# Performance work log

Measured on AMD Instinct MI355X. Metric: run time of the kernel, lower is better.

Reference implementation:

```python
import jax, jax.numpy as jnp
import numpy as np

B, S, D = 4, 4096, 1024
E, H, TOPK = 8, 2752, 2


def setup_inputs() -> dict:
    key = jax.random.key(0)
    k0, k1, k2, k3, k4 = jax.random.split(key, 5)
    x = jax.random.normal(k0, (B, S, D), dtype=jnp.float32)
    gate_w = jax.random.normal(k1, (E, D), dtype=jnp.float32) * 0.02
    w1 = jax.random.normal(k2, (E, H, D), dtype=jnp.float32) * 0.02
    w2 = jax.random.normal(k3, (E, D, H), dtype=jnp.float32) * 0.02
    w3 = jax.random.normal(k4, (E, H, D), dtype=jnp.float32) * 0.02
    return {"x": x, "gate_w": gate_w, "w1": w1, "w2": w2, "w3": w3}


def reference(x, gate_w, w1, w2, w3):
    """MoE layer: softmax router -> top-k (normalized) -> per-expert SwiGLU FFN -> weighted combine."""
    b, s, d = x.shape
    xt = x.reshape(-1, d)                       # [T, D], T = B*S
    logits = xt @ gate_w.T                      # [T, E]
    scores = jax.nn.softmax(logits, axis=-1)
    topk_w, topk_i = jax.lax.top_k(scores, TOPK)  # [T, K]
    topk_w = topk_w / (jnp.sum(topk_w, axis=-1, keepdims=True) + 1e-20)

    y = jnp.zeros_like(xt)
    n_experts = gate_w.shape[0]
    for e in range(n_experts):
        # combine weight for expert e per token (0 if not routed to e)
        we = jnp.sum(jnp.where(topk_i == e, topk_w, 0.0), axis=-1)  # [T]
        h = jax.nn.silu(xt @ w1[e].T) * (xt @ w3[e].T)              # [T, H]
        y = y + we[:, None] * (h @ w2[e].T)                         # [T, D]
    return y.reshape(b, s, d)
```

## Files before the change

### kernel.cpp

```cpp
#include <hip/hip_runtime.h>
#include <hip/hip_bf16.h>
#include <stdint.h>

#define T_TOK 16384
#define D_DIM 1024
#define E_NUM 8
#define H_DIM 2752
#define NSLOT (T_TOK * 2)

typedef __bf16 bf16x8_t __attribute__((ext_vector_type(8)));
typedef float f32x4_t __attribute__((ext_vector_type(4)));

__device__ __forceinline__ uint16_t f2bf(float f) {
    union { float f; uint32_t u; } v; v.f = f;
    return (uint16_t)((v.u + 0x7FFFu + ((v.u >> 16) & 1u)) >> 16);
}
__device__ __forceinline__ ushort4 f4_to_bf4(float4 v) {
    ushort4 r; r.x = f2bf(v.x); r.y = f2bf(v.y); r.z = f2bf(v.z); r.w = f2bf(v.w);
    return r;
}
__device__ __forceinline__ void gl_lds16(const uint16_t* g, uint16_t* l) {
    __builtin_amdgcn_global_load_lds((const __attribute__((address_space(1))) void*)g,
                                     (__attribute__((address_space(3))) void*)l,
                                     16, 0, 0);
}

__global__ __launch_bounds__(256) void router_kernel(
    const float* __restrict__ x, const float* __restrict__ gw,
    int* __restrict__ topk_i, float* __restrict__ topk_w) {
    int tid = threadIdx.x;
    int t = blockIdx.x * 4 + (tid >> 6);
    int lane = tid & 63;
    const float* xr = x + (size_t)t * D_DIM;
    double acc[E_NUM];
#pragma unroll
    for (int e = 0; e < E_NUM; ++e) acc[e] = 0.0;
    for (int k = lane; k < D_DIM; k += 64) {
        double xv = (double)xr[k];
#pragma unroll
        for (int e = 0; e < E_NUM; ++e) acc[e] += xv * (double)gw[e * D_DIM + k];
    }
#pragma unroll
    for (int e = 0; e < E_NUM; ++e) {
        double v = acc[e];
        for (int off = 32; off > 0; off >>= 1) v += __shfl_down(v, off, 64);
        acc[e] = v;
    }
    if (lane == 0) {
        int i0 = 0; double m0 = acc[0];
#pragma unroll
        for (int e = 1; e < E_NUM; ++e) if (acc[e] > m0) { m0 = acc[e]; i0 = e; }
        int i1 = -1; double m1 = -1.0e300;
#pragma unroll
        for (int e = 0; e < E_NUM; ++e) if (e != i0 && acc[e] > m1) { m1 = acc[e]; i1 = e; }
        double e1 = exp(m1 - m0);
        double s = 1.0 + e1;
        topk_i[t * 2 + 0] = i0; topk_i[t * 2 + 1] = i1;
        topk_w[t * 2 + 0] = (float)(1.0 / s);
        topk_w[t * 2 + 1] = (float)(e1 / s);
    }
}

__global__ __launch_bounds__(256) void count_kernel(
    const int* __restrict__ topk_i,
    int* __restrict__ counts_f, int* __restrict__ counts_s) {
    __shared__ int hf[E_NUM], hs[E_NUM];
    int tid = threadIdx.x;
    if (tid < E_NUM) { hf[tid] = 0; hs[tid] = 0; }
    __syncthreads();
    int t = blockIdx.x * 256 + tid;
    atomicAdd(&hf[topk_i[t * 2 + 0]], 1);
    atomicAdd(&hs[topk_i[t * 2 + 1]], 1);
    __syncthreads();
    if (tid < E_NUM) {
        if (hf[tid]) atomicAdd(&counts_f[tid], hf[tid]);
    } else if (tid < 2 * E_NUM) {
        int e = tid - E_NUM;
        if (hs[e]) atomicAdd(&counts_s[e], hs[e]);
    }
}

__global__ void prefix_kernel(const int* __restrict__ cf, const int* __restrict__ cs,
                              int* __restrict__ bases, int* __restrict__ splits,
                              int* __restrict__ cnts) {
    int s = 0;
    for (int e = 0; e < E_NUM; ++e) {
        bases[e] = s;
        splits[e] = s + cf[e];
        cnts[e] = cf[e] + cs[e];
        s += cnts[e];
    }
}

__global__ __launch_bounds__(256) void assign_kernel(
    const int* __restrict__ topk_i, const float* __restrict__ topk_w,
    const int* __restrict__ bases, const int* __restrict__ splits,
    int* __restrict__ fills_f, int* __restrict__ fills_s,
    int* __restrict__ slot_tok, float* __restrict__ slot_w) {
    __shared__ int hf[E_NUM], hs[E_NUM], bf[E_NUM], bs[E_NUM];
    int tid = threadIdx.x;
    if (tid < E_NUM) { hf[tid] = 0; hs[tid] = 0; }
    __syncthreads();
    int t = blockIdx.x * 256 + tid;
    int e0 = topk_i[t * 2 + 0], e1 = topk_i[t * 2 + 1];
    int r0 = atomicAdd(&hf[e0], 1);
    int r1 = atomicAdd(&hs[e1], 1);
    __syncthreads();
    if (tid < E_NUM) {
        bf[tid] = hf[tid] ? atomicAdd(&fills_f[tid], hf[tid]) : 0;
    } else if (tid < 2 * E_NUM) {
        int e = tid - E_NUM;
        bs[e] = hs[e] ? atomicAdd(&fills_s[e], hs[e]) : 0;
    }
    __syncthreads();
    int s0 = bases[e0] + bf[e0] + r0;
    int s1 = splits[e1] + bs[e1] + r1;
    slot_tok[s0] = t; slot_w[s0] = topk_w[t * 2 + 0];
    slot_tok[s1] = t; slot_w[s1] = topk_w[t * 2 + 1];
}

__global__ __launch_bounds__(256) void cvtx_kernel(const float* __restrict__ x,
                                                   uint16_t* __restrict__ Xb) {
    size_t i = (size_t)blockIdx.x * 256 + threadIdx.x;
    ((ushort4*)Xb)[i] = f4_to_bf4(((const float4*)x)[i]);
}
__global__ __launch_bounds__(256) void cvt13g_kernel(const float* __restrict__ w1,
                                                     const float* __restrict__ w3,
                                                     uint16_t* __restrict__ w1be,
                                                     uint16_t* __restrict__ w3be, int g) {
    size_t i = (size_t)blockIdx.x * 256 + threadIdx.x;
    size_t off = (size_t)g * 4 * H_DIM * D_DIM / 4;
    ((ushort4*)w1be)[i] = f4_to_bf4(((const float4*)w1)[off + i]);
    ((ushort4*)w3be)[i] = f4_to_bf4(((const float4*)w3)[off + i]);
}
__global__ __launch_bounds__(256) void cvt2_kernel(const float* __restrict__ w2,
                                                   uint16_t* __restrict__ w2b) {
    size_t i = (size_t)blockIdx.x * 256 + threadIdx.x;
    ((ushort4*)w2b)[i] = f4_to_bf4(((const float4*)w2)[i]);
}


__global__ __launch_bounds__(256) void gemm1_kernel(
    const uint16_t* __restrict__ Xb, const uint16_t* __restrict__ w1be,
    const uint16_t* __restrict__ w3be, const int* __restrict__ slot_tok,
    const int* __restrict__ cnts, const int* __restrict__ bases,
    uint16_t* __restrict__ hidden, int g) {
    int ez = blockIdx.z;
    int e = g * 4 + ez;
    int cnt = cnts[e];
    int m0 = blockIdx.y * 128;
    if (m0 >= cnt) return;
    int n0 = blockIdx.x * 64;
    int base = bases[e];
    const uint16_t* w1p = w1be + (size_t)ez * H_DIM * D_DIM;
    const uint16_t* w3p = w3be + (size_t)ez * H_DIM * D_DIM;

    __shared__ __align__(16) uint16_t As[128 * 64];
    __shared__ __align__(16) uint16_t B1s[64 * 64];
    __shared__ __align__(16) uint16_t B3s[64 * 64];

    int tid = threadIdx.x;
    int w = tid >> 6, lane = tid & 63;
    int rA = lane & 15, kq = lane >> 4;
    int r8 = lane >> 3;
    int srcc = (lane & 7) ^ ((w * 4 + (lane >> 4)) & 7);
    int xr = (rA >> 1) & 7;

    const uint16_t *pA0, *pA1, *pA2, *pA3, *pB1, *pB3;
    {
        int sr = w * 8 + r8;
        int t0 = slot_tok[base + min(m0 + 0 * 32 + sr, cnt - 1)];
        int t1 = slot_tok[base + min(m0 + 1 * 32 + sr, cnt - 1)];
        int t2 = slot_tok[base + min(m0 + 2 * 32 + sr, cnt - 1)];
        int t3 = slot_tok[base + min(m0 + 3 * 32 + sr, cnt - 1)];
        pA0 = Xb + (size_t)t0 * D_DIM + srcc * 8;
        pA1 = Xb + (size_t)t1 * D_DIM + srcc * 8;
        pA2 = Xb + (size_t)t2 * D_DIM + srcc * 8;
        pA3 = Xb + (size_t)t3 * D_DIM + srcc * 8;
        pB1 = w1p + (size_t)(n0 + sr) * D_DIM + srcc * 8;
        pB3 = w3p + (size_t)(n0 + sr) * D_DIM + srcc * 8;
    }
    uint16_t* lA = &As[(w * 8) * 64];
    uint16_t* lB1 = &B1s[(w * 8) * 64];
    uint16_t* lB3 = &B3s[(w * 8) * 64];

    f32x4_t acc1[2][4], acc3[2][4];
#pragma unroll
    for (int r = 0; r < 2; ++r)
#pragma unroll
        for (int n = 0; n < 4; ++n) {
            acc1[r][n] = (f32x4_t){0.f, 0.f, 0.f, 0.f};
            acc3[r][n] = (f32x4_t){0.f, 0.f, 0.f, 0.f};
        }

    for (int k0 = 0; k0 < D_DIM; k0 += 64) {
        __syncthreads();
        gl_lds16(pA0, lA);
        gl_lds16(pA1, lA + 32 * 64);
        gl_lds16(pA2, lA + 64 * 64);
        gl_lds16(pA3, lA + 96 * 64);
        gl_lds16(pB1, lB1);
        gl_lds16(pB1 + 32 * D_DIM, lB1 + 32 * 64);
        gl_lds16(pB3, lB3);
        gl_lds16(pB3 + 32 * D_DIM, lB3 + 32 * 64);
        pA0 += 64; pA1 += 64; pA2 += 64; pA3 += 64; pB1 += 64; pB3 += 64;
        __syncthreads();

#pragma unroll
        for (int kk = 0; kk < 2; ++kk) {
            int ck = ((kk * 4 + kq) ^ xr) * 8;
            bf16x8_t a0 = *(const bf16x8_t*)&As[(w * 32 + rA) * 64 + ck];
            bf16x8_t a1 = *(const bf16x8_t*)&As[(w * 32 + 16 + rA) * 64 + ck];
#pragma unroll
            for (int n = 0; n < 4; ++n) {
                bf16x8_t b1 = *(const bf16x8_t*)&B1s[(n * 16 + rA) * 64 + ck];
                bf16x8_t b3 = *(const bf16x8_t*)&B3s[(n * 16 + rA) * 64 + ck];
                acc1[0][n] = __builtin_amdgcn_mfma_f32_16x16x32_bf16(a0, b1, acc1[0][n], 0, 0, 0);
                acc1[1][n] = __builtin_amdgcn_mfma_f32_16x16x32_bf16(a1, b1, acc1[1][n], 0, 0, 0);
                acc3[0][n] = __builtin_amdgcn_mfma_f32_16x16x32_bf16(a0, b3, acc3[0][n], 0, 0, 0);
                acc3[1][n] = __builtin_amdgcn_mfma_f32_16x16x32_bf16(a1, b3, acc3[1][n], 0, 0, 0);
            }
        }
    }

#pragma unroll
    for (int r = 0; r < 2; ++r)
#pragma unroll
        for (int n = 0; n < 4; ++n)
#pragma unroll
            for (int i = 0; i < 4; ++i) {
                int mrow = m0 + w * 32 + r * 16 + kq * 4 + i;
                if (mrow < cnt) {
                    float gv = acc1[r][n][i];
                    float s = gv / (1.0f + __expf(-gv));
                    float h = s * acc3[r][n][i];
                    hidden[(size_t)(base + mrow) * H_DIM + n0 + n * 16 + rA] = f2bf(h);
                }
            }
}

__global__ __launch_bounds__(256) void gemm2_kernel(
    const uint16_t* __restrict__ hidden, const uint16_t* __restrict__ w2b,
    const int* __restrict__ cnts, const int* __restrict__ bases,
    const int* __restrict__ slot_tok, const float* __restrict__ slot_w,
    float* __restrict__ out) {
    int e = blockIdx.z;
    int cnt = cnts[e];
    int lin = blockIdx.y * 8 + blockIdx.x;
    int c8 = lin & 7, j = lin >> 3;
    int m_t = (j >> 3) * 8 + c8;
    int x_t = j & 7;
    int m0 = m_t * 128;
    if (m0 >= cnt) return;
    int base = bases[e];
    int d0 = x_t * 128;

    __shared__ __align__(16) uint16_t As[128 * 64];
    __shared__ __align__(16) uint16_t Bs[128 * 64];

    int tid = threadIdx.x;
    int w = tid >> 6, lane = tid & 63;
    int rA = lane & 15, kq = lane >> 4;
    int r8 = lane >> 3;
    int srcc = (lane & 7) ^ ((w * 4 + (lane >> 4)) & 7);
    int xr = (rA >> 1) & 7;
    int mh = w & 1, nh = w >> 1;

    const uint16_t *pA0, *pA1, *pA2, *pA3, *pB;
    {
        int sr = w * 8 + r8;
        int s0 = base + min(m0 + 0 * 32 + sr, cnt - 1);
        int s1 = base + min(m0 + 1 * 32 + sr, cnt - 1);
        int s2 = base + min(m0 + 2 * 32 + sr, cnt - 1);
        int s3 = base + min(m0 + 3 * 32 + sr, cnt - 1);
        pA0 = hidden + (size_t)s0 * H_DIM + srcc * 8;
        pA1 = hidden + (size_t)s1 * H_DIM + srcc * 8;
        pA2 = hidden + (size_t)s2 * H_DIM + srcc * 8;
        pA3 = hidden + (size_t)s3 * H_DIM + srcc * 8;
        pB = w2b + (size_t)(e * D_DIM + d0 + sr) * H_DIM + srcc * 8;
    }
    uint16_t* lA = &As[(w * 8) * 64];
    uint16_t* lB = &Bs[(w * 8) * 64];

    f32x4_t acc[4][4];
#pragma unroll
    for (int mf = 0; mf < 4; ++mf)
#pragma unroll
        for (int nf = 0; nf < 4; ++nf) acc[mf][nf] = (f32x4_t){0.f, 0.f, 0.f, 0.f};

    for (int k0 = 0; k0 < H_DIM; k0 += 64) {
        __syncthreads();
        gl_lds16(pA0, lA);
        gl_lds16(pA1, lA + 32 * 64);
        gl_lds16(pA2, lA + 64 * 64);
        gl_lds16(pA3, lA + 96 * 64);
        gl_lds16(pB, lB);
        gl_lds16(pB + 32 * H_DIM, lB + 32 * 64);
        gl_lds16(pB + 64 * H_DIM, lB + 64 * 64);
        gl_lds16(pB + 96 * H_DIM, lB + 96 * 64);
        pA0 += 64; pA1 += 64; pA2 += 64; pA3 += 64; pB += 64;
        __syncthreads();

#pragma unroll
        for (int kk = 0; kk < 2; ++kk) {
            int ck = ((kk * 4 + kq) ^ xr) * 8;
            bf16x8_t a[4], b[4];
#pragma unroll
            for (int mf = 0; mf < 4; ++mf)
                a[mf] = *(const bf16x8_t*)&As[(mh * 64 + mf * 16 + rA) * 64 + ck];
#pragma unroll
            for (int nf = 0; nf < 4; ++nf)
                b[nf] = *(const bf16x8_t*)&Bs[(nh * 64 + nf * 16 + rA) * 64 + ck];
#pragma unroll
            for (int mf = 0; mf < 4; ++mf)
#pragma unroll
                for (int nf = 0; nf < 4; ++nf)
                    acc[mf][nf] = __builtin_amdgcn_mfma_f32_16x16x32_bf16(a[mf], b[nf], acc[mf][nf], 0, 0, 0);
        }
    }

#pragma unroll
    for (int mf = 0; mf < 4; ++mf)
#pragma unroll
        for (int i = 0; i < 4; ++i) {
            int mr = m0 + mh * 64 + mf * 16 + kq * 4 + i;
            if (mr < cnt) {
                int slot = base + mr;
                float wgt = slot_w[slot];
                int tok = slot_tok[slot];
                float* yr = out + (size_t)tok * D_DIM + d0 + nh * 64;
#pragma unroll
                for (int nf = 0; nf < 4; ++nf)
                    atomicAdd(&yr[nf * 16 + rA], wgt * acc[mf][nf][i]);
            }
        }
}

extern "C" void kernel_launch(void* const* d_in, const int* in_sizes, int n_in,
                              void* d_out, int out_size, void* d_ws, size_t ws_size,
                              hipStream_t stream) {
    const float* x  = (const float*)d_in[0];
    const float* gw = (const float*)d_in[1];
    const float* w1 = (const float*)d_in[2];
    const float* w2 = (const float*)d_in[3];
    const float* w3 = (const float*)d_in[4];
    float* out = (float*)d_out;
    char* ws = (char*)d_ws;

    int*   counts_f = (int*)(ws + 0);
    int*   counts_s = (int*)(ws + 256);
    int*   fills_f  = (int*)(ws + 512);
    int*   fills_s  = (int*)(ws + 768);
    int*   bases    = (int*)(ws + 1024);
    int*   splits   = (int*)(ws + 1280);
    int*   cnts     = (int*)(ws + 1536);
    int*   topk_i   = (int*)(ws + 4096);
    float* topk_w   = (float*)(ws + 4096 + 1 * 131072);
    int*   slot_tok = (int*)(ws + 4096 + 2 * 131072);
    float* slot_w   = (float*)(ws + 4096 + 3 * 131072);

    const size_t HID_OFF = 4ull << 20;
    const size_t W_OFF   = HID_OFF + (size_t)NSLOT * H_DIM * 2;
    const size_t W1SZ    = (size_t)H_DIM * D_DIM * 2;
    uint16_t* hidden = (uint16_t*)(ws + HID_OFF);
    uint16_t* w1be   = (uint16_t*)(ws + W_OFF);
    uint16_t* w3be   = (uint16_t*)(ws + W_OFF + 4 * W1SZ);
    uint16_t* w2b    = (uint16_t*)(ws + W_OFF);
    uint16_t* Xb     = (uint16_t*)d_out;

    hipMemsetAsync(ws, 0, 1024, stream);

    router_kernel<<<T_TOK / 4, 256, 0, stream>>>(x, gw, topk_i, topk_w);
    count_kernel<<<T_TOK / 256, 256, 0, stream>>>(topk_i, counts_f, counts_s);
    prefix_kernel<<<1, 1, 0, stream>>>(counts_f, counts_s, bases, splits, cnts);
    assign_kernel<<<T_TOK / 256, 256, 0, stream>>>(topk_i, topk_w, bases, splits,
                                                   fills_f, fills_s, slot_tok, slot_w);
    cvtx_kernel<<<T_TOK * D_DIM / 1024, 256, 0, stream>>>(x, Xb);

    for (int g = 0; g < 2; ++g) {
        cvt13g_kernel<<<H_DIM * 4, 256, 0, stream>>>(w1, w3, w1be, w3be, g);
        gemm1_kernel<<<dim3(H_DIM / 64, 128, 4), 256, 0, stream>>>(
            Xb, w1be, w3be, slot_tok, cnts, bases, hidden, g);
    }

    hipMemsetAsync(out, 0, (size_t)T_TOK * D_DIM * sizeof(float), stream);
    cvt2_kernel<<<E_NUM * D_DIM * H_DIM / 1024, 256, 0, stream>>>(w2, w2b);
    gemm2_kernel<<<dim3(8, 128, E_NUM), 256, 0, stream>>>(
        hidden, w2b, cnts, bases, slot_tok, slot_w, out);
}
```

Before: 1.198 ms.

## Enlarge GEMM M-tiles to 256 rows with 512-thread blocks and fuse x conversion into router

Both expert GEMMs now use 512-thread blocks covering 256 token rows, arranged as a 4x2 wave grid, so each weight tile loaded into LDS is reused across twice as many tokens. The grids shrink to match. The separate x-to-bf16 conversion kernel is removed, and the router, which already reads each row of x, now writes the bf16 copy. The larger tiles raise LDS use and register pressure per block, and they add more padded rows for experts whose token count is not a multiple of 256.

```diff
diff --git a/kernel.cpp b/kernel.cpp
--- a/kernel.cpp
+++ b/kernel.cpp
@@ -27,7 +27,8 @@
 
 __global__ __launch_bounds__(256) void router_kernel(
     const float* __restrict__ x, const float* __restrict__ gw,
-    int* __restrict__ topk_i, float* __restrict__ topk_w) {
+    int* __restrict__ topk_i, float* __restrict__ topk_w,
+    uint16_t* __restrict__ Xb) {
     int tid = threadIdx.x;
     int t = blockIdx.x * 4 + (tid >> 6);
     int lane = tid & 63;
@@ -39,6 +40,12 @@
         double xv = (double)xr[k];
 #pragma unroll
         for (int e = 0; e < E_NUM; ++e) acc[e] += xv * (double)gw[e * D_DIM + k];
+    }
+    {
+        const float4* x4 = (const float4*)xr;
+        ushort4* b4 = (ushort4*)(Xb + (size_t)t * D_DIM);
+#pragma unroll
+        for (int j = 0; j < 4; ++j) b4[lane + j * 64] = f4_to_bf4(x4[lane + j * 64]);
     }
 #pragma unroll
     for (int e = 0; e < E_NUM; ++e) {
@@ -119,11 +126,6 @@
     slot_tok[s1] = t; slot_w[s1] = topk_w[t * 2 + 1];
 }
 
-__global__ __launch_bounds__(256) void cvtx_kernel(const float* __restrict__ x,
-                                                   uint16_t* __restrict__ Xb) {
-    size_t i = (size_t)blockIdx.x * 256 + threadIdx.x;
-    ((ushort4*)Xb)[i] = f4_to_bf4(((const float4*)x)[i]);
-}
 __global__ __launch_bounds__(256) void cvt13g_kernel(const float* __restrict__ w1,
                                                      const float* __restrict__ w3,
                                                      uint16_t* __restrict__ w1be,
@@ -140,7 +142,7 @@
 }
 
 
-__global__ __launch_bounds__(256) void gemm1_kernel(
+__global__ __launch_bounds__(512, 4) void gemm1_kernel(
     const uint16_t* __restrict__ Xb, const uint16_t* __restrict__ w1be,
     const uint16_t* __restrict__ w3be, const int* __restrict__ slot_tok,
     const int* __restrict__ cnts, const int* __restrict__ bases,
@@ -148,31 +150,31 @@
     int ez = blockIdx.z;
     int e = g * 4 + ez;
     int cnt = cnts[e];
-    int m0 = blockIdx.y * 128;
+    int m0 = blockIdx.y * 256;
     if (m0 >= cnt) return;
     int n0 = blockIdx.x * 64;
     int base = bases[e];
     const uint16_t* w1p = w1be + (size_t)ez * H_DIM * D_DIM;
     const uint16_t* w3p = w3be + (size_t)ez * H_DIM * D_DIM;
 
-    __shared__ __align__(16) uint16_t As[128 * 64];
+    __shared__ __align__(16) uint16_t As[256 * 64];
     __shared__ __align__(16) uint16_t B1s[64 * 64];
     __shared__ __align__(16) uint16_t B3s[64 * 64];
 
     int tid = threadIdx.x;
     int w = tid >> 6, lane = tid & 63;
+    int wm = w >> 1, wn = w & 1;
     int rA = lane & 15, kq = lane >> 4;
-    int r8 = lane >> 3;
     int srcc = (lane & 7) ^ ((w * 4 + (lane >> 4)) & 7);
     int xr = (rA >> 1) & 7;
 
     const uint16_t *pA0, *pA1, *pA2, *pA3, *pB1, *pB3;
     {
-        int sr = w * 8 + r8;
-        int t0 = slot_tok[base + min(m0 + 0 * 32 + sr, cnt - 1)];
-        int t1 = slot_tok[base + min(m0 + 1 * 32 + sr, cnt - 1)];
-        int t2 = slot_tok[base + min(m0 + 2 * 32 + sr, cnt - 1)];
-        int t3 = slot_tok[base + min(m0 + 3 * 32 + sr, cnt - 1)];
+        int sr = w * 8 + (lane >> 3);
+        int t0 = slot_tok[base + min(m0 + 0 * 64 + sr, cnt - 1)];
+        int t1 = slot_tok[base + min(m0 + 1 * 64 + sr, cnt - 1)];
+        int t2 = slot_tok[base + min(m0 + 2 * 64 + sr, cnt - 1)];
+        int t3 = slot_tok[base + min(m0 + 3 * 64 + sr, cnt - 1)];
         pA0 = Xb + (size_t)t0 * D_DIM + srcc * 8;
         pA1 = Xb + (size_t)t1 * D_DIM + srcc * 8;
         pA2 = Xb + (size_t)t2 * D_DIM + srcc * 8;
@@ -180,66 +182,72 @@
         pB1 = w1p + (size_t)(n0 + sr) * D_DIM + srcc * 8;
         pB3 = w3p + (size_t)(n0 + sr) * D_DIM + srcc * 8;
     }
-    uint16_t* lA = &As[(w * 8) * 64];
+    uint16_t* lA0 = &As[(0 * 64 + w * 8) * 64];
+    uint16_t* lA1 = &As[(1 * 64 + w * 8) * 64];
+    uint16_t* lA2 = &As[(2 * 64 + w * 8) * 64];
+    uint16_t* lA3 = &As[(3 * 64 + w * 8) * 64];
     uint16_t* lB1 = &B1s[(w * 8) * 64];
     uint16_t* lB3 = &B3s[(w * 8) * 64];
 
-    f32x4_t acc1[2][4], acc3[2][4];
-#pragma unroll
-    for (int r = 0; r < 2; ++r)
-#pragma unroll
-        for (int n = 0; n < 4; ++n) {
-            acc1[r][n] = (f32x4_t){0.f, 0.f, 0.f, 0.f};
-            acc3[r][n] = (f32x4_t){0.f, 0.f, 0.f, 0.f};
+    f32x4_t acc1[4][2], acc3[4][2];
+#pragma unroll
+    for (int mf = 0; mf < 4; ++mf)
+#pragma unroll
+        for (int nf = 0; nf < 2; ++nf) {
+            acc1[mf][nf] = (f32x4_t){0.f, 0.f, 0.f, 0.f};
+            acc3[mf][nf] = (f32x4_t){0.f, 0.f, 0.f, 0.f};
         }
 
     for (int k0 = 0; k0 < D_DIM; k0 += 64) {
         __syncthreads();
-        gl_lds16(pA0, lA);
-        gl_lds16(pA1, lA + 32 * 64);
-        gl_lds16(pA2, lA + 64 * 64);
-        gl_lds16(pA3, lA + 96 * 64);
+        gl_lds16(pA0, lA0);
+        gl_lds16(pA1, lA1);
+        gl_lds16(pA2, lA2);
+        gl_lds16(pA3, lA3);
         gl_lds16(pB1, lB1);
-        gl_lds16(pB1 + 32 * D_DIM, lB1 + 32 * 64);
         gl_lds16(pB3, lB3);
-        gl_lds16(pB3 + 32 * D_DIM, lB3 + 32 * 64);
         pA0 += 64; pA1 += 64; pA2 += 64; pA3 += 64; pB1 += 64; pB3 += 64;
         __syncthreads();
 
 #pragma unroll
         for (int kk = 0; kk < 2; ++kk) {
             int ck = ((kk * 4 + kq) ^ xr) * 8;
-            bf16x8_t a0 = *(const bf16x8_t*)&As[(w * 32 + rA) * 64 + ck];
-            bf16x8_t a1 = *(const bf16x8_t*)&As[(w * 32 + 16 + rA) * 64 + ck];
-#pragma unroll
-            for (int n = 0; n < 4; ++n) {
-                bf16x8_t b1 = *(const bf16x8_t*)&B1s[(n * 16 + rA) * 64 + ck];
-                bf16x8_t b3 = *(const bf16x8_t*)&B3s[(n * 16 + rA) * 64 + ck];
-                acc1[0][n] = __builtin_amdgcn_mfma_f32_16x16x32_bf16(a0, b1, acc1[0][n], 0, 0, 0);
-                acc1[1][n] = __builtin_amdgcn_mfma_f32_16x16x32_bf16(a1, b1, acc1[1][n], 0, 0, 0);
-                acc3[0][n] = __builtin_amdgcn_mfma_f32_16x16x32_bf16(a0, b3, acc3[0][n], 0, 0, 0);
-                acc3[1][n] = __builtin_amdgcn_mfma_f32_16x16x32_bf16(a1, b3, acc3[1][n], 0, 0, 0);
+            bf16x8_t a[4], b1[2], b3[2];
+#pragma unroll
+            for (int mf = 0; mf < 4; ++mf)
+                a[mf] = *(const bf16x8_t*)&As[(wm * 64 + mf * 16 + rA) * 64 + ck];
+#pragma unroll
+            for (int nf = 0; nf < 2; ++nf) {
+                b1[nf] = *(const bf16x8_t*)&B1s[(wn * 32 + nf * 16 + rA) * 64 + ck];
+                b3[nf] = *(const bf16x8_t*)&B3s[(wn * 32 + nf * 16 + rA) * 64 + ck];
             }
+#pragma unroll
+            for (int mf = 0; mf < 4; ++mf)
+#pragma unroll
+                for (int nf = 0; nf < 2; ++nf) {
+                    acc1[mf][nf] = __builtin_amdgcn_mfma_f32_16x16x32_bf16(a[mf], b1[nf], acc1[mf][nf], 0, 0, 0);
+                    acc3[mf][nf] = __builtin_amdgcn_mfma_f32_16x16x32_bf16(a[mf], b3[nf], acc3[mf][nf], 0, 0, 0);
+                }
         }
     }
 
 #pragma unroll
-    for (int r = 0; r < 2; ++r)
-#pragma unroll
-        for (int n = 0; n < 4; ++n)
+    for (int mf = 0; mf < 4; ++mf)
+#pragma unroll
+        for (int nf = 0; nf < 2; ++nf)
 #pragma unroll
             for (int i = 0; i < 4; ++i) {
-                int mrow = m0 + w * 32 + r * 16 + kq * 4 + i;
+                int mrow = m0 + wm * 64 + mf * 16 + kq * 4 + i;
                 if (mrow < cnt) {
-                    float gv = acc1[r][n][i];
+                    float gv = acc1[mf][nf][i];
                     float s = gv / (1.0f + __expf(-gv));
-                    float h = s * acc3[r][n][i];
-                    hidden[(size_t)(base + mrow) * H_DIM + n0 + n * 16 + rA] = f2bf(h);
+                    float h = s * acc3[mf][nf][i];
+                    hidden[(size_t)(base + mrow) * H_DIM + n0 + wn * 32 + nf * 16 + rA] = f2bf(h);
                 }
             }
 }
 
-__global__ __launch_bounds__(256) void gemm2_kernel(
+__global__ __launch_bounds__(512, 4) void gemm2_kernel(
     const uint16_t* __restrict__ hidden, const uint16_t* __restrict__ w2b,
     const int* __restrict__ cnts, const int* __restrict__ bases,
     const int* __restrict__ slot_tok, const float* __restrict__ slot_w,
@@ -250,37 +258,41 @@
     int c8 = lin & 7, j = lin >> 3;
     int m_t = (j >> 3) * 8 + c8;
     int x_t = j & 7;
-    int m0 = m_t * 128;
+    int m0 = m_t * 256;
     if (m0 >= cnt) return;
     int base = bases[e];
     int d0 = x_t * 128;
 
-    __shared__ __align__(16) uint16_t As[128 * 64];
+    __shared__ __align__(16) uint16_t As[256 * 64];
     __shared__ __align__(16) uint16_t Bs[128 * 64];
 
     int tid = threadIdx.x;
     int w = tid >> 6, lane = tid & 63;
+    int wm = w >> 1, wn = w & 1;
     int rA = lane & 15, kq = lane >> 4;
-    int r8 = lane >> 3;
     int srcc = (lane & 7) ^ ((w * 4 + (lane >> 4)) & 7);
     int xr = (rA >> 1) & 7;
-    int mh = w & 1, nh = w >> 1;
-
-    const uint16_t *pA0, *pA1, *pA2, *pA3, *pB;
+
+    const uint16_t *pA0, *pA1, *pA2, *pA3, *pB0, *pB1;
     {
-        int sr = w * 8 + r8;
-        int s0 = base + min(m0 + 0 * 32 + sr, cnt - 1);
-        int s1 = base + min(m0 + 1 * 32 + sr, cnt - 1);
-        int s2 = base + min(m0 + 2 * 32 + sr, cnt - 1);
-        int s3 = base + min(m0 + 3 * 32 + sr, cnt - 1);
+        int sr = w * 8 + (lane >> 3);
+        int s0 = base + min(m0 + 0 * 64 + sr, cnt - 1);
+        int s1 = base + min(m0 + 1 * 64 + sr, cnt - 1);
+        int s2 = base + min(m0 + 2 * 64 + sr, cnt - 1);
+        int s3 = base + min(m0 + 3 * 64 + sr, cnt - 1);
         pA0 = hidden + (size_t)s0 * H_DIM + srcc * 8;
         pA1 = hidden + (size_t)s1 * H_DIM + srcc * 8;
         pA2 = hidden + (size_t)s2 * H_DIM + srcc * 8;
         pA3 = hidden + (size_t)s3 * H_DIM + srcc * 8;
-        pB = w2b + (size_t)(e * D_DIM + d0 + sr) * H_DIM + srcc * 8;
-    }
-    uint16_t* lA = &As[(w * 8) * 64];
-    uint16_t* lB = &Bs[(w * 8) * 64];
+        pB0 = w2b + (size_t)(e * D_DIM + d0 + 0 * 64 + sr) * H_DIM + srcc * 8;
+        pB1 = w2b + (size_t)(e * D_DIM + d0 + 1 * 64 + sr) * H_DIM + srcc * 8;
+    }
+    uint16_t* lA0 = &As[(0 * 64 + w * 8) * 64];
+    uint16_t* lA1 = &As[(1 * 64 + w * 8) * 64];
+    uint16_t* lA2 = &As[(2 * 64 + w * 8) * 64];
+    uint16_t* lA3 = &As[(3 * 64 + w * 8) * 64];
+    uint16_t* lB0 = &Bs[(0 * 64 + w * 8) * 64];
+    uint16_t* lB1 = &Bs[(1 * 64 + w * 8) * 64];
 
     f32x4_t acc[4][4];
 #pragma unroll
@@ -290,15 +302,13 @@
 
     for (int k0 = 0; k0 < H_DIM; k0 += 64) {
         __syncthreads();
-        gl_lds16(pA0, lA);
-        gl_lds16(pA1, lA + 32 * 64);
-        gl_lds16(pA2, lA + 64 * 64);
-        gl_lds16(pA3, lA + 96 * 64);
-        gl_lds16(pB, lB);
-        gl_lds16(pB + 32 * H_DIM, lB + 32 * 64);
-        gl_lds16(pB + 64 * H_DIM, lB + 64 * 64);
-        gl_lds16(pB + 96 * H_DIM, lB + 96 * 64);
-        pA0 += 64; pA1 += 64; pA2 += 64; pA3 += 64; pB += 64;
+        gl_lds16(pA0, lA0);
+        gl_lds16(pA1, lA1);
+        gl_lds16(pA2, lA2);
+        gl_lds16(pA3, lA3);
+        gl_lds16(pB0, lB0);
+        gl_lds16(pB1, lB1);
+        pA0 += 64; pA1 += 64; pA2 += 64; pA3 += 64; pB0 += 64; pB1 += 64;
         __syncthreads();
 
 #pragma unroll
@@ -307,10 +317,10 @@
             bf16x8_t a[4], b[4];
 #pragma unroll
             for (int mf = 0; mf < 4; ++mf)
-                a[mf] = *(const bf16x8_t*)&As[(mh * 64 + mf * 16 + rA) * 64 + ck];
+                a[mf] = *(const bf16x8_t*)&As[(wm * 64 + mf * 16 + rA) * 64 + ck];
 #pragma unroll
             for (int nf = 0; nf < 4; ++nf)
-                b[nf] = *(const bf16x8_t*)&Bs[(nh * 64 + nf * 16 + rA) * 64 + ck];
+                b[nf] = *(const bf16x8_t*)&Bs[(wn * 64 + nf * 16 + rA) * 64 + ck];
 #pragma unroll
             for (int mf = 0; mf < 4; ++mf)
 #pragma unroll
@@ -323,12 +333,12 @@
     for (int mf = 0; mf < 4; ++mf)
 #pragma unroll
         for (int i = 0; i < 4; ++i) {
-            int mr = m0 + mh * 64 + mf * 16 + kq * 4 + i;
+            int mr = m0 + wm * 64 + mf * 16 + kq * 4 + i;
             if (mr < cnt) {
                 int slot = base + mr;
                 float wgt = slot_w[slot];
                 int tok = slot_tok[slot];
-                float* yr = out + (size_t)tok * D_DIM + d0 + nh * 64;
+                float* yr = out + (size_t)tok * D_DIM + d0 + wn * 64;
 #pragma unroll
                 for (int nf = 0; nf < 4; ++nf)
                     atomicAdd(&yr[nf * 16 + rA], wgt * acc[mf][nf][i]);
@@ -370,21 +380,20 @@
 
     hipMemsetAsync(ws, 0, 1024, stream);
 
-    router_kernel<<<T_TOK / 4, 256, 0, stream>>>(x, gw, topk_i, topk_w);
+    router_kernel<<<T_TOK / 4, 256, 0, stream>>>(x, gw, topk_i, topk_w, Xb);
     count_kernel<<<T_TOK / 256, 256, 0, stream>>>(topk_i, counts_f, counts_s);
     prefix_kernel<<<1, 1, 0, stream>>>(counts_f, counts_s, bases, splits, cnts);
     assign_kernel<<<T_TOK / 256, 256, 0, stream>>>(topk_i, topk_w, bases, splits,
                                                    fills_f, fills_s, slot_tok, slot_w);
-    cvtx_kernel<<<T_TOK * D_DIM / 1024, 256, 0, stream>>>(x, Xb);
 
     for (int g = 0; g < 2; ++g) {
         cvt13g_kernel<<<H_DIM * 4, 256, 0, stream>>>(w1, w3, w1be, w3be, g);
-        gemm1_kernel<<<dim3(H_DIM / 64, 128, 4), 256, 0, stream>>>(
+        gemm1_kernel<<<dim3(H_DIM / 64, 64, 4), 512, 0, stream>>>(
             Xb, w1be, w3be, slot_tok, cnts, bases, hidden, g);
     }
 
     hipMemsetAsync(out, 0, (size_t)T_TOK * D_DIM * sizeof(float), stream);
     cvt2_kernel<<<E_NUM * D_DIM * H_DIM / 1024, 256, 0, stream>>>(w2, w2b);
-    gemm2_kernel<<<dim3(8, 128, E_NUM), 256, 0, stream>>>(
+    gemm2_kernel<<<dim3(8, 64, E_NUM), 512, 0, stream>>>(
         hidden, w2b, cnts, bases, slot_tok, slot_w, out);
 }
```

Result: slower. 1.317 ms (+9.9%).

## Fuse x bf16 conversion into router and flatten GEMM grid ordering

Applied to the files above, without the earlier changes.

Folds the fp32-to-bf16 conversion of x into the router kernel, which already reads each token row, and removes the separate cvtx kernel launch and its second read of x. It also remaps the GEMM grids so that experts and column tiles share blockIdx.x while the row tile uses blockIdx.y. This changes block dispatch order, so blocks working on the same row tile of one expert launch together, and for gemm2 it drops the earlier swizzled tile mapping. The goal is better L2 reuse of the activation tiles and fewer early-exit blocks scattered through the launch order. The tradeoff is losing the weight-tile locality the old swizzle gave.

```diff
diff --git a/kernel.cpp b/kernel.cpp
--- a/kernel.cpp
+++ b/kernel.cpp
@@ -27,7 +27,8 @@
 
 __global__ __launch_bounds__(256) void router_kernel(
     const float* __restrict__ x, const float* __restrict__ gw,
-    int* __restrict__ topk_i, float* __restrict__ topk_w) {
+    int* __restrict__ topk_i, float* __restrict__ topk_w,
+    uint16_t* __restrict__ Xb) {
     int tid = threadIdx.x;
     int t = blockIdx.x * 4 + (tid >> 6);
     int lane = tid & 63;
@@ -39,6 +40,12 @@
         double xv = (double)xr[k];
 #pragma unroll
         for (int e = 0; e < E_NUM; ++e) acc[e] += xv * (double)gw[e * D_DIM + k];
+    }
+    {
+        const float4* x4 = (const float4*)xr;
+        ushort4* b4 = (ushort4*)(Xb + (size_t)t * D_DIM);
+#pragma unroll
+        for (int j = 0; j < 4; ++j) b4[lane + j * 64] = f4_to_bf4(x4[lane + j * 64]);
     }
 #pragma unroll
     for (int e = 0; e < E_NUM; ++e) {
@@ -119,11 +126,6 @@
     slot_tok[s1] = t; slot_w[s1] = topk_w[t * 2 + 1];
 }
 
-__global__ __launch_bounds__(256) void cvtx_kernel(const float* __restrict__ x,
-                                                   uint16_t* __restrict__ Xb) {
-    size_t i = (size_t)blockIdx.x * 256 + threadIdx.x;
-    ((ushort4*)Xb)[i] = f4_to_bf4(((const float4*)x)[i]);
-}
 __global__ __launch_bounds__(256) void cvt13g_kernel(const float* __restrict__ w1,
                                                      const float* __restrict__ w3,
                                                      uint16_t* __restrict__ w1be,
@@ -145,12 +147,13 @@
     const uint16_t* __restrict__ w3be, const int* __restrict__ slot_tok,
     const int* __restrict__ cnts, const int* __restrict__ bases,
     uint16_t* __restrict__ hidden, int g) {
-    int ez = blockIdx.z;
+    int ez = blockIdx.x / 43;
+    int n_t = blockIdx.x % 43;
     int e = g * 4 + ez;
     int cnt = cnts[e];
     int m0 = blockIdx.y * 128;
     if (m0 >= cnt) return;
-    int n0 = blockIdx.x * 64;
+    int n0 = n_t * 64;
     int base = bases[e];
     const uint16_t* w1p = w1be + (size_t)ez * H_DIM * D_DIM;
     const uint16_t* w3p = w3be + (size_t)ez * H_DIM * D_DIM;
@@ -244,13 +247,10 @@
     const int* __restrict__ cnts, const int* __restrict__ bases,
     const int* __restrict__ slot_tok, const float* __restrict__ slot_w,
     float* __restrict__ out) {
-    int e = blockIdx.z;
+    int x_t = blockIdx.x & 7;
+    int e = blockIdx.x >> 3;
     int cnt = cnts[e];
-    int lin = blockIdx.y * 8 + blockIdx.x;
-    int c8 = lin & 7, j = lin >> 3;
-    int m_t = (j >> 3) * 8 + c8;
-    int x_t = j & 7;
-    int m0 = m_t * 128;
+    int m0 = blockIdx.y * 128;
     if (m0 >= cnt) return;
     int base = bases[e];
     int d0 = x_t * 128;
@@ -370,21 +370,20 @@
 
     hipMemsetAsync(ws, 0, 1024, stream);
 
-    router_kernel<<<T_TOK / 4, 256, 0, stream>>>(x, gw, topk_i, topk_w);
+    router_kernel<<<T_TOK / 4, 256, 0, stream>>>(x, gw, topk_i, topk_w, Xb);
     count_kernel<<<T_TOK / 256, 256, 0, stream>>>(topk_i, counts_f, counts_s);
     prefix_kernel<<<1, 1, 0, stream>>>(counts_f, counts_s, bases, splits, cnts);
     assign_kernel<<<T_TOK / 256, 256, 0, stream>>>(topk_i, topk_w, bases, splits,
                                                    fills_f, fills_s, slot_tok, slot_w);
-    cvtx_kernel<<<T_TOK * D_DIM / 1024, 256, 0, stream>>>(x, Xb);
 
     for (int g = 0; g < 2; ++g) {
         cvt13g_kernel<<<H_DIM * 4, 256, 0, stream>>>(w1, w3, w1be, w3be, g);
-        gemm1_kernel<<<dim3(H_DIM / 64, 128, 4), 256, 0, stream>>>(
+        gemm1_kernel<<<dim3(172, 128), 256, 0, stream>>>(
             Xb, w1be, w3be, slot_tok, cnts, bases, hidden, g);
     }
 
     hipMemsetAsync(out, 0, (size_t)T_TOK * D_DIM * sizeof(float), stream);
     cvt2_kernel<<<E_NUM * D_DIM * H_DIM / 1024, 256, 0, stream>>>(w2, w2b);
-    gemm2_kernel<<<dim3(8, 128, E_NUM), 256, 0, stream>>>(
+    gemm2_kernel<<<dim3(64, 128), 256, 0, stream>>>(
         hidden, w2b, cnts, bases, slot_tok, slot_w, out);
 }
```

New measurement: 1.211 ms. Within noise of the previous version (+1.1%).
